# Optimization experiments

Measured on AMD Instinct MI355X. Metric: run time of the kernel, lower is better.

## Reference

```python
import jax, jax.numpy as jnp
import numpy as np

B, N, DM, H, DH, DI = 32, 512, 512, 8, 64, 2048
LEAKY_SLOPE = 0.01  # torch F.leaky_relu default
EPS = 1e-5          # torch LayerNorm default


def _ln(x, w, b):
    mu = jnp.mean(x, axis=-1, keepdims=True)
    var = jnp.var(x, axis=-1, keepdims=True)
    return (x - mu) * jax.lax.rsqrt(var + EPS) * w + b


def setup_inputs() -> dict:
    key = jax.random.key(0)
    ks = jax.random.split(key, 12)
    s = 0.02
    return {
        "Z": jax.random.normal(ks[0], (B, N, DM), jnp.float32),
        "D": jax.random.uniform(ks[1], (B, N, N), jnp.float32) * 10.0,  # pairwise distances
        "new_mask": jnp.zeros((B, N, N), jnp.float32),   # additive pre-softmax mask
        "mask": jnp.ones((B, N, N), jnp.float32),        # multiplicative post-softmax mask
        "gamma": jnp.ones((4, 4), jnp.float32),          # region-pair bias table
        "qkv_w": jax.random.normal(ks[2], (3 * DM, DM), jnp.float32) * s,
        "qkv_b": jnp.zeros((3 * DM,), jnp.float32),
        "o_w": jax.random.normal(ks[3], (DM, H * DH), jnp.float32) * s,
        "ln1_w": jnp.ones((DM,), jnp.float32),
        "ln1_b": jnp.zeros((DM,), jnp.float32),
        "ln2_w": jnp.ones((DM,), jnp.float32),
        "ln2_b": jnp.zeros((DM,), jnp.float32),
        "p1_w": jax.random.normal(ks[4], (DI, DM), jnp.float32) * s,
        "p1_b": jnp.zeros((DI,), jnp.float32),
        "p2_w": jax.random.normal(ks[5], (DM, DI), jnp.float32) * s,
        "p2_b": jnp.zeros((DM,), jnp.float32),
        "ra_end": 170,  # RA = slice(0,170), RB = slice(170,340), RT = slice(340,N)
        "rb_end": 340,
    }


def reference(Z, D, new_mask, mask, gamma, qkv_w, qkv_b, o_w,
              ln1_w, ln1_b, ln2_w, ln2_b, p1_w, p1_b, p2_w, p2_b,
              ra_end, rb_end):
    bsz, n, dm = Z.shape
    # region id per element: 0=RA, 1=RB, 2=RT (use_quad=False)
    idx = jnp.arange(n)
    region = (idx >= ra_end).astype(jnp.int32) + (idx >= rb_end).astype(jnp.int32)
    gamma_mask = gamma[region[:, None], region[None, :]]  # [N, N]

    inp = Z
    Zn = _ln(Z, ln1_w, ln1_b)
    qkv = (Zn @ qkv_w.T + qkv_b).reshape(bsz, n, H, 3 * DH)
    Z2, Z3, Z4 = jnp.split(qkv, 3, axis=3)  # V, Q, K : [B,N,H,DH]

    # scores[b,h,n,m] = -gamma*D + QK/sqrt(d) + additive mask
    scores = (-(gamma_mask[None] * D)[:, None]
              + jnp.einsum('bnhd,bmhd->bhnm', Z3, Z4) / np.sqrt(DH)
              + new_mask[:, None])
    W = jax.nn.softmax(scores, axis=3) * mask[:, None]  # post-softmax masking

    attn = jnp.einsum('bhnm,bmhd->bnhd', W, Z2).reshape(bsz, n, dm)
    attn = jax.nn.leaky_relu(attn, LEAKY_SLOPE) @ o_w.T  # o_net has no bias
    Z = attn + inp

    inp2 = Z
    Zn2 = _ln(Z, ln2_w, ln2_b)
    return jax.nn.relu(Zn2 @ p1_w.T + p1_b) @ p2_w.T + p2_b + inp2
```

## Files before the change

kernel.cpp:

```cpp
#include <hip/hip_runtime.h>
#include <hip/hip_bf16.h>

#define B_  32
#define N_  512
#define DM_ 512
#define H_  8
#define DH_ 64
#define DI_ 2048

typedef __attribute__((ext_vector_type(8))) __bf16 bf16x8;
typedef __attribute__((ext_vector_type(4))) float f32x4;
typedef __attribute__((ext_vector_type(8))) unsigned short us8;
typedef __attribute__((ext_vector_type(4))) unsigned short us4;
typedef __attribute__((ext_vector_type(4))) unsigned int u32x4;

typedef __attribute__((address_space(1))) const void g_cvoid;
typedef __attribute__((address_space(3))) void l_void;

__device__ __forceinline__ float b2f(unsigned short u) {
  union { unsigned int i; float f; } x; x.i = ((unsigned int)u) << 16; return x.f;
}
__device__ __forceinline__ unsigned short f2b(float f) {
  union { float f; unsigned int i; } x; x.f = f;
  unsigned int r = x.i + 0x7FFFu + ((x.i >> 16) & 1u);
  return (unsigned short)(r >> 16);
}
__device__ __forceinline__ void gld_lds16(const unsigned short* g, unsigned short* l) {
  __builtin_amdgcn_global_load_lds((g_cvoid*)g, (l_void*)l, 16, 0, 0);
}

__global__ __launch_bounds__(256) void prep_sm(const float* __restrict__ Dg,
                                               const float* __restrict__ nmg,
                                               const float* __restrict__ mkg,
                                               const float* __restrict__ gammaf,
                                               const int* __restrict__ ra,
                                               const int* __restrict__ rb,
                                               unsigned int* __restrict__ packed) {
  __shared__ unsigned int t[64][65];
  const int bid = blockIdx.x;
  const int kt = bid & 7, qt = (bid >> 3) & 7, b = bid >> 6;
  const int tid = threadIdx.x;
  const int ra_e = *ra, rb_e = *rb;
  const int r = tid >> 2;
  const int c = (tid & 3) * 16;
  const int q_g = qt * 64 + r;
  const int rq = (q_g >= ra_e) + (q_g >= rb_e);
  const float g0 = gammaf[rq * 4], g1 = gammaf[rq * 4 + 1], g2 = gammaf[rq * 4 + 2];
  const size_t base = ((size_t)b * N_ + q_g) * N_ + kt * 64 + c;
#pragma unroll
  for (int i = 0; i < 4; i++) {
    f32x4 dv = *(const f32x4*)(Dg + base + i * 4);
    f32x4 nv = *(const f32x4*)(nmg + base + i * 4);
    f32x4 mv = *(const f32x4*)(mkg + base + i * 4);
#pragma unroll
    for (int j = 0; j < 4; j++) {
      const int gk = kt * 64 + c + i * 4 + j;
      const float g = gk >= rb_e ? g2 : (gk >= ra_e ? g1 : g0);
      const float E = __expf(nv[j] - g * dv[j]);
      const float Em = E * mv[j];
      t[r][c + i * 4 + j] = (unsigned int)f2b(E) | ((unsigned int)f2b(Em) << 16);
    }
  }
  __syncthreads();
  const int rr = tid >> 2;
  const int cc = (tid & 3) * 16;
  unsigned int* dst = packed + ((size_t)b * N_ + kt * 64 + rr) * N_ + qt * 64 + cc;
#pragma unroll
  for (int i = 0; i < 4; i++) {
    u32x4 v;
#pragma unroll
    for (int j = 0; j < 4; j++) v[j] = t[cc + i * 4 + j][rr];
    *(u32x4*)(dst + i * 4) = v;
  }
}

__global__ __launch_bounds__(256) void conv_w(const float* __restrict__ a, const float* __restrict__ b,
                                              const float* __restrict__ c, const float* __restrict__ d,
                                              unsigned short* __restrict__ oa, unsigned short* __restrict__ ob,
                                              unsigned short* __restrict__ oc, unsigned short* __restrict__ od) {
  const int bid = blockIdx.x;
  const float* src; unsigned short* dst; int idx;
  if (bid < 384)       { src = a; dst = oa; idx = bid; }
  else if (bid < 512)  { src = b; dst = ob; idx = bid - 384; }
  else if (bid < 1024) { src = c; dst = oc; idx = bid - 512; }
  else                 { src = d; dst = od; idx = bid - 1024; }
  const int off = idx * 2048 + threadIdx.x * 8;
  f32x4 x0 = *(const f32x4*)(src + off);
  f32x4 x1 = *(const f32x4*)(src + off + 4);
  us8 o;
#pragma unroll
  for (int i = 0; i < 4; i++) { o[i] = f2b(x0[i]); o[4 + i] = f2b(x1[i]); }
  *(us8*)(dst + off) = o;
}

__global__ __launch_bounds__(256) void ln_kernel(const float* __restrict__ x,
                                                 const float* __restrict__ w,
                                                 const float* __restrict__ b,
                                                 unsigned short* __restrict__ y) {
  const int row  = blockIdx.x * 4 + (threadIdx.x >> 6);
  const int lane = threadIdx.x & 63;
  const float* xr = x + (size_t)row * DM_ + lane * 8;
  f32x4 x0 = *(const f32x4*)xr;
  f32x4 x1 = *(const f32x4*)(xr + 4);
  float v[8]; float s = 0.f;
#pragma unroll
  for (int i = 0; i < 4; i++) { v[i] = x0[i]; v[4 + i] = x1[i]; }
#pragma unroll
  for (int i = 0; i < 8; i++) s += v[i];
#pragma unroll
  for (int o = 1; o < 64; o <<= 1) s += __shfl_xor(s, o);
  const float mu = s * (1.f / DM_);
  float q = 0.f;
#pragma unroll
  for (int i = 0; i < 8; i++) { float d = v[i] - mu; q += d * d; }
#pragma unroll
  for (int o = 1; o < 64; o <<= 1) q += __shfl_xor(q, o);
  const float rstd = rsqrtf(q * (1.f / DM_) + 1e-5f);
  f32x4 w0 = *(const f32x4*)(w + lane * 8);
  f32x4 w1 = *(const f32x4*)(w + lane * 8 + 4);
  f32x4 b0 = *(const f32x4*)(b + lane * 8);
  f32x4 b1 = *(const f32x4*)(b + lane * 8 + 4);
  us8 out;
#pragma unroll
  for (int i = 0; i < 4; i++) {
    out[i]     = f2b((v[i] - mu) * rstd * w0[i] + b0[i]);
    out[4 + i] = f2b((v[4 + i] - mu) * rstd * w1[i] + b1[i]);
  }
  *(us8*)(y + (size_t)row * DM_ + lane * 8) = out;
}

struct GemmP {
  const unsigned short* A;
  const unsigned short* Bw;
  const float* bias;
  const float* residf;
  unsigned short* outb;
  float* outf;
  unsigned short* out_q;
  unsigned short* out_k;
  int K;
  int tiles_n;
  int ldo;
};

template <int EPI>
__global__ __launch_bounds__(256) void gemm_bt(GemmP p) {
  __shared__ unsigned short As[128 * 32];
  __shared__ unsigned short Bs[128 * 32];
  const int tid = threadIdx.x;
  const int wave = tid >> 6, lane = tid & 63;
  const int wm = wave >> 1, wn = wave & 1;
  const int tn = blockIdx.x % p.tiles_n, tm = blockIdx.x / p.tiles_n;
  const int K = p.K;
  const unsigned short* Ab = p.A + (size_t)tm * 128 * K;
  const unsigned short* Bb = p.Bw + (size_t)tn * 128 * K;
  f32x4 acc[4][4];
#pragma unroll
  for (int i = 0; i < 4; i++)
#pragma unroll
    for (int j = 0; j < 4; j++) acc[i][j] = (f32x4){0.f, 0.f, 0.f, 0.f};

  const int srow = lane >> 2;
  const int scol = (lane & 3) * 8;
  for (int kt = 0; kt < K; kt += 32) {
    __syncthreads();
#pragma unroll
    for (int i = 0; i < 2; i++) {
      const int r = wave * 32 + i * 16;
      gld_lds16(Ab + (size_t)(r + srow) * K + kt + scol, &As[r * 32]);
      gld_lds16(Bb + (size_t)(r + srow) * K + kt + scol, &Bs[r * 32]);
    }
    __syncthreads();
    bf16x8 af[4], bfr[4];
#pragma unroll
    for (int m = 0; m < 4; m++)
      af[m] = *(const bf16x8*)&As[(wm * 64 + m * 16 + (lane & 15)) * 32 + (lane >> 4) * 8];
#pragma unroll
    for (int n = 0; n < 4; n++)
      bfr[n] = *(const bf16x8*)&Bs[(wn * 64 + n * 16 + (lane & 15)) * 32 + (lane >> 4) * 8];
#pragma unroll
    for (int m = 0; m < 4; m++)
#pragma unroll
      for (int n = 0; n < 4; n++)
        acc[m][n] = __builtin_amdgcn_mfma_f32_16x16x32_bf16(af[m], bfr[n], acc[m][n], 0, 0, 0);
  }

  const int r0 = tm * 128 + wm * 64;
  const int c0 = tn * 128 + wn * 64;
#pragma unroll
  for (int m = 0; m < 4; m++) {
#pragma unroll
    for (int n = 0; n < 4; n++) {
#pragma unroll
      for (int rr = 0; rr < 4; rr++) {
        const int row = r0 + m * 16 + (lane >> 4) * 4 + rr;
        const int col = c0 + n * 16 + (lane & 15);
        float v = acc[m][n][rr];
        if (EPI == 0) {
          v += p.bias[col];
          const int h = col / 192, j = col % 192;
          const int bb = row >> 9, nn = row & 511;
          const size_t base = (((size_t)bb * H_ + h) * N_ + nn) * DH_;
          if (j < 64)       p.outb [base + j]        = f2b(v);
          else if (j < 128) p.out_q[base + j - 64]   = f2b(v * 0.125f);
          else              p.out_k[base + j - 128]  = f2b(v);
        } else if (EPI == 1) {
          p.outf[(size_t)row * p.ldo + col] = v + p.residf[(size_t)row * p.ldo + col];
        } else if (EPI == 2) {
          v += p.bias[col];
          v = v > 0.f ? v : 0.f;
          p.outb[(size_t)row * p.ldo + col] = f2b(v);
        } else {
          p.outf[(size_t)row * p.ldo + col] =
              v + p.bias[col] + p.residf[(size_t)row * p.ldo + col];
        }
      }
    }
  }
}

__global__ __launch_bounds__(256) void transp_v(const unsigned short* __restrict__ V,
                                                unsigned short* __restrict__ Vt) {
  __shared__ unsigned short t[64][65];
  const int bid = blockIdx.x;
  const int bh = bid >> 3, nt = bid & 7;
  const int n0 = nt * 64;
  const int tid = threadIdx.x;
  const unsigned short* src = V + ((size_t)bh * N_ + n0) * DH_;
  {
    const int r = tid >> 2, c = (tid & 3) * 16;
    us8 a = *(const us8*)(src + (size_t)r * DH_ + c);
    us8 b8 = *(const us8*)(src + (size_t)r * DH_ + c + 8);
#pragma unroll
    for (int i = 0; i < 8; i++) { t[r][c + i] = a[i]; t[r][c + 8 + i] = b8[i]; }
  }
  __syncthreads();
  {
    const int d = tid >> 2, nc = (tid & 3) * 16;
    us8 o1, o2;
#pragma unroll
    for (int i = 0; i < 8; i++) { o1[i] = t[nc + i][d]; o2[i] = t[nc + 8 + i][d]; }
    unsigned short* dst = Vt + ((size_t)bh * DH_ + d) * N_ + n0 + nc;
    *(us8*)dst = o1;
    *(us8*)(dst + 8) = o2;
  }
}

__global__ __launch_bounds__(256, 3) void attn_kernel(
    const unsigned short* __restrict__ Qs, const unsigned short* __restrict__ Ks,
    const unsigned short* __restrict__ Vt, const unsigned int* __restrict__ packed,
    unsigned short* __restrict__ attn_out) {
  __shared__ unsigned short Kt[64 * 64];
  __shared__ unsigned short Vtt[64 * 64];

  const int bid = blockIdx.x;
  const int qt = bid & 7, h = (bid >> 3) & 7, b = bid >> 6;
  const int q0 = qt * 64;
  const int tid = threadIdx.x, wave = tid >> 6, lane = tid & 63;
  const int q = lane & 15, hi = lane >> 4;

  const int q_g = q0 + wave * 16 + q;
  const size_t bh = (size_t)b * H_ + h;
  const unsigned short* Qb = Qs + (bh * N_ + q_g) * DH_;
  bf16x8 qf[2];
  qf[0] = *(const bf16x8*)(Qb + hi * 8);
  qf[1] = *(const bf16x8*)(Qb + 32 + hi * 8);

  const unsigned short* Kb = Ks + bh * N_ * DH_;
  const unsigned short* Vb = Vt + bh * DH_ * N_;
  const unsigned int* Pb = packed + (size_t)b * N_ * N_ + (size_t)(hi * 4) * N_ + q_g - wave * 16 - q
                           + (q0 + wave * 16 + q) - q0 - wave * 16 - q + q0 + wave * 16 + q;
  const unsigned int* Pbase = packed + (size_t)b * N_ * N_ + q_g;

  f32x4 o[4];
#pragma unroll
  for (int i = 0; i < 4; i++) o[i] = (f32x4){0.f, 0.f, 0.f, 0.f};
  float dsum = 0.f;

  const int str = tid >> 2;
  const int stc = tid & 3;

  us8 pk0, pk1, pv0, pv1;
  unsigned int ppw[16];

  auto load_tile = [&](int kt) {
    const unsigned short* Kp = Kb + (size_t)(kt + str) * DH_ + stc * 16;
    const unsigned short* Vp = Vb + (size_t)str * N_ + kt + stc * 16;
    pk0 = *(const us8*)Kp;
    pk1 = *(const us8*)(Kp + 8);
    pv0 = *(const us8*)Vp;
    pv1 = *(const us8*)(Vp + 8);
    const unsigned int* Pp = Pbase + (size_t)(kt + hi * 4) * N_;
#pragma unroll
    for (int c = 0; c < 4; c++)
#pragma unroll
      for (int j = 0; j < 4; j++)
        ppw[c * 4 + j] = Pp[(size_t)(c * 16 + j) * N_];
  };

  load_tile(0);

  for (int kt = 0; kt < N_; kt += 64) {
    __syncthreads();
    {
      const int c0 = (stc * 2) ^ (str & 7);
      const int c1 = (stc * 2 + 1) ^ (str & 7);
      *(us8*)&Kt[str * 64 + c0 * 8] = pk0;
      *(us8*)&Kt[str * 64 + c1 * 8] = pk1;
      *(us8*)&Vtt[str * 64 + c0 * 8] = pv0;
      *(us8*)&Vtt[str * 64 + c1 * 8] = pv1;
    }
    unsigned int cpw[16];
#pragma unroll
    for (int i = 0; i < 16; i++) cpw[i] = ppw[i];
    __syncthreads();
    if (kt + 64 < N_) load_tile(kt + 64);

    f32x4 s4[4];
#pragma unroll
    for (int c = 0; c < 4; c++) {
      f32x4 a = (f32x4){0.f, 0.f, 0.f, 0.f};
#pragma unroll
      for (int kd = 0; kd < 2; kd++) {
        const int krow = c * 16 + q;
        const int chunk = (kd * 4 + hi) ^ (q & 7);
        bf16x8 kf = *(const bf16x8*)&Kt[krow * 64 + chunk * 8];
        a = __builtin_amdgcn_mfma_f32_16x16x32_bf16(kf, qf[kd], a, 0, 0, 0);
      }
      s4[c] = a;
    }

    unsigned int pkk[4][2];
#pragma unroll
    for (int c = 0; c < 4; c++) {
      float pm[4];
#pragma unroll
      for (int r = 0; r < 4; r++) {
        const float es = __expf(s4[c][r]);
        const unsigned int w = cpw[c * 4 + r];
        dsum += es * b2f((unsigned short)(w & 0xffffu));
        pm[r] = es * b2f((unsigned short)(w >> 16));
      }
      pkk[c][0] = (unsigned int)f2b(pm[0]) | ((unsigned int)f2b(pm[1]) << 16);
      pkk[c][1] = (unsigned int)f2b(pm[2]) | ((unsigned int)f2b(pm[3]) << 16);
    }

#pragma unroll
    for (int dc = 0; dc < 4; dc++) {
      const int vrow = dc * 16 + q;
#pragma unroll
      for (int t = 0; t < 2; t++) {
        u32x4 pb = {pkk[t][0], pkk[t][1], pkk[t + 2][0], pkk[t + 2][1]};
        bf16x8 pf = __builtin_bit_cast(bf16x8, pb);
        const int ch1 = (2 * t + (hi >> 1)) ^ (vrow & 7);
        const int ch2 = (2 * t + 4 + (hi >> 1)) ^ (vrow & 7);
        us4 v1 = *(const us4*)&Vtt[vrow * 64 + ch1 * 8 + (hi & 1) * 4];
        us4 v2 = *(const us4*)&Vtt[vrow * 64 + ch2 * 8 + (hi & 1) * 4];
        us8 vv;
#pragma unroll
        for (int i = 0; i < 4; i++) { vv[i] = v1[i]; vv[4 + i] = v2[i]; }
        bf16x8 vf = __builtin_bit_cast(bf16x8, vv);
        o[dc] = __builtin_amdgcn_mfma_f32_16x16x32_bf16(vf, pf, o[dc], 0, 0, 0);
      }
    }
  }

  dsum += __shfl_xor(dsum, 16);
  dsum += __shfl_xor(dsum, 32);
  const float inv = 1.f / dsum;

  const size_t obase = ((size_t)b * N_ + q_g) * DM_ + h * DH_ + hi * 4;
#pragma unroll
  for (int dc = 0; dc < 4; dc++) {
    us4 ov;
#pragma unroll
    for (int r = 0; r < 4; r++) {
      float val = o[dc][r] * inv;
      val = val >= 0.f ? val : 0.01f * val;
      ov[r] = f2b(val);
    }
    *(us4*)&attn_out[obase + dc * 16] = ov;
  }
}

extern "C" void kernel_launch(void* const* d_in, const int* in_sizes, int n_in,
                              void* d_out, int out_size, void* d_ws, size_t ws_size,
                              hipStream_t stream) {
  const float* Z     = (const float*)d_in[0];
  const float* D     = (const float*)d_in[1];
  const float* nm    = (const float*)d_in[2];
  const float* mask  = (const float*)d_in[3];
  const float* gamma = (const float*)d_in[4];
  const float* qkv_w = (const float*)d_in[5];
  const float* qkv_b = (const float*)d_in[6];
  const float* o_w   = (const float*)d_in[7];
  const float* ln1_w = (const float*)d_in[8];
  const float* ln1_b = (const float*)d_in[9];
  const float* ln2_w = (const float*)d_in[10];
  const float* ln2_b = (const float*)d_in[11];
  const float* p1_w  = (const float*)d_in[12];
  const float* p1_b  = (const float*)d_in[13];
  const float* p2_w  = (const float*)d_in[14];
  const float* p2_b  = (const float*)d_in[15];
  const int* ra = (const int*)d_in[16];
  const int* rb = (const int*)d_in[17];
  float* out = (float*)d_out;

  const size_t SZ = (size_t)16384 * 512;
  unsigned short* buf0  = (unsigned short*)d_ws;
  unsigned short* bufQ  = buf0 + SZ;
  unsigned short* bufK  = bufQ + SZ;
  unsigned short* bufV  = bufK + SZ;
  unsigned short* bufVt = bufV + SZ;
  float* bufZ = (float*)(bufVt + SZ);
  unsigned short* bufH = bufQ;
  unsigned int* packed = (unsigned int*)bufZ;
  unsigned short* wQKV = (unsigned short*)(bufZ + SZ);
  unsigned short* wO   = wQKV + (size_t)3 * DM_ * DM_;
  unsigned short* wP1  = wO + (size_t)DM_ * DM_;
  unsigned short* wP2  = wP1 + (size_t)DI_ * DM_;

  prep_sm<<<2048, 256, 0, stream>>>(D, nm, mask, gamma, ra, rb, packed);

  conv_w<<<1536, 256, 0, stream>>>(qkv_w, o_w, p1_w, p2_w, wQKV, wO, wP1, wP2);

  ln_kernel<<<4096, 256, 0, stream>>>(Z, ln1_w, ln1_b, buf0);

  GemmP p1{};
  p1.A = buf0; p1.Bw = wQKV; p1.bias = qkv_b;
  p1.outb = bufV; p1.out_q = bufQ; p1.out_k = bufK;
  p1.K = 512; p1.tiles_n = 12; p1.ldo = 0;
  gemm_bt<0><<<128 * 12, 256, 0, stream>>>(p1);

  transp_v<<<2048, 256, 0, stream>>>(bufV, bufVt);

  attn_kernel<<<B_ * H_ * 8, 256, 0, stream>>>(bufQ, bufK, bufVt, packed, buf0);

  GemmP p3{};
  p3.A = buf0; p3.Bw = wO; p3.residf = Z; p3.outf = bufZ;
  p3.K = 512; p3.tiles_n = 4; p3.ldo = 512;
  gemm_bt<1><<<128 * 4, 256, 0, stream>>>(p3);

  ln_kernel<<<4096, 256, 0, stream>>>(bufZ, ln2_w, ln2_b, buf0);

  GemmP p5{};
  p5.A = buf0; p5.Bw = wP1; p5.bias = p1_b; p5.outb = bufH;
  p5.K = 512; p5.tiles_n = 16; p5.ldo = 2048;
  gemm_bt<2><<<128 * 16, 256, 0, stream>>>(p5);

  GemmP p6{};
  p6.A = bufH; p6.Bw = wP2; p6.bias = p2_b; p6.residf = bufZ; p6.outf = out;
  p6.K = 2048; p6.tiles_n = 4; p6.ldo = 512;
  gemm_bt<3><<<128 * 4, 256, 0, stream>>>(p6);
}
```

Measured before the change: 323.1 us.

## Double-buffer GEMM LDS staging and add XCD-aware block swizzle

The bf16 GEMM kernel now keeps two LDS buffers for the A and B tiles. It issues the global-to-LDS loads for the next K slice before running the MFMAs on the current one, and uses one barrier per iteration instead of two, so load latency overlaps with compute. Both the GEMM and attention kernels remap blockIdx so that consecutive logical tiles land on the same XCD, aiming for better L2 reuse of shared weight and K/V tiles. The swizzle assumes the grid size is a multiple of 8. The double buffer doubles GEMM shared memory, which may lower occupancy. A dead pointer computation in the attention kernel is also removed.

New measurement: 289.1 us. 10.5% less time.

```diff
diff --git a/kernel.cpp b/kernel.cpp
--- a/kernel.cpp
+++ b/kernel.cpp
@@ -27,6 +27,9 @@
 }
 __device__ __forceinline__ void gld_lds16(const unsigned short* g, unsigned short* l) {
   __builtin_amdgcn_global_load_lds((g_cvoid*)g, (l_void*)l, 16, 0, 0);
+}
+__device__ __forceinline__ int xcd_swz(int bid, int nwg) {
+  return (bid & 7) * (nwg >> 3) + (bid >> 3);
 }
 
 __global__ __launch_bounds__(256) void prep_sm(const float* __restrict__ Dg,
@@ -145,12 +148,13 @@
 
 template <int EPI>
 __global__ __launch_bounds__(256) void gemm_bt(GemmP p) {
-  __shared__ unsigned short As[128 * 32];
-  __shared__ unsigned short Bs[128 * 32];
+  __shared__ unsigned short As[2][128 * 32];
+  __shared__ unsigned short Bs[2][128 * 32];
   const int tid = threadIdx.x;
   const int wave = tid >> 6, lane = tid & 63;
   const int wm = wave >> 1, wn = wave & 1;
-  const int tn = blockIdx.x % p.tiles_n, tm = blockIdx.x / p.tiles_n;
+  const int bid = xcd_swz(blockIdx.x, gridDim.x);
+  const int tn = bid % p.tiles_n, tm = bid / p.tiles_n;
   const int K = p.K;
   const unsigned short* Ab = p.A + (size_t)tm * 128 * K;
   const unsigned short* Bb = p.Bw + (size_t)tn * 128 * K;
@@ -162,27 +166,34 @@
 
   const int srow = lane >> 2;
   const int scol = (lane & 3) * 8;
-  for (int kt = 0; kt < K; kt += 32) {
-    __syncthreads();
+  auto stage = [&](int buf, int kt) {
 #pragma unroll
     for (int i = 0; i < 2; i++) {
       const int r = wave * 32 + i * 16;
-      gld_lds16(Ab + (size_t)(r + srow) * K + kt + scol, &As[r * 32]);
-      gld_lds16(Bb + (size_t)(r + srow) * K + kt + scol, &Bs[r * 32]);
-    }
-    __syncthreads();
+      gld_lds16(Ab + (size_t)(r + srow) * K + kt + scol, &As[buf][r * 32]);
+      gld_lds16(Bb + (size_t)(r + srow) * K + kt + scol, &Bs[buf][r * 32]);
+    }
+  };
+
+  stage(0, 0);
+  __syncthreads();
+  const int nIter = K >> 5;
+  for (int it = 0; it < nIter; it++) {
+    const int buf = it & 1;
+    if (it + 1 < nIter) stage(buf ^ 1, (it + 1) * 32);
     bf16x8 af[4], bfr[4];
 #pragma unroll
     for (int m = 0; m < 4; m++)
-      af[m] = *(const bf16x8*)&As[(wm * 64 + m * 16 + (lane & 15)) * 32 + (lane >> 4) * 8];
+      af[m] = *(const bf16x8*)&As[buf][(wm * 64 + m * 16 + (lane & 15)) * 32 + (lane >> 4) * 8];
 #pragma unroll
     for (int n = 0; n < 4; n++)
-      bfr[n] = *(const bf16x8*)&Bs[(wn * 64 + n * 16 + (lane & 15)) * 32 + (lane >> 4) * 8];
+      bfr[n] = *(const bf16x8*)&Bs[buf][(wn * 64 + n * 16 + (lane & 15)) * 32 + (lane >> 4) * 8];
 #pragma unroll
     for (int m = 0; m < 4; m++)
 #pragma unroll
       for (int n = 0; n < 4; n++)
         acc[m][n] = __builtin_amdgcn_mfma_f32_16x16x32_bf16(af[m], bfr[n], acc[m][n], 0, 0, 0);
+    __syncthreads();
   }
 
   const int r0 = tm * 128 + wm * 64;
@@ -253,7 +264,7 @@
   __shared__ unsigned short Kt[64 * 64];
   __shared__ unsigned short Vtt[64 * 64];
 
-  const int bid = blockIdx.x;
+  const int bid = xcd_swz(blockIdx.x, gridDim.x);
   const int qt = bid & 7, h = (bid >> 3) & 7, b = bid >> 6;
   const int q0 = qt * 64;
   const int tid = threadIdx.x, wave = tid >> 6, lane = tid & 63;
@@ -268,8 +279,6 @@
 
   const unsigned short* Kb = Ks + bh * N_ * DH_;
   const unsigned short* Vb = Vt + bh * DH_ * N_;
-  const unsigned int* Pb = packed + (size_t)b * N_ * N_ + (size_t)(hi * 4) * N_ + q_g - wave * 16 - q
-                           + (q0 + wave * 16 + q) - q0 - wave * 16 - q + q0 + wave * 16 + q;
   const unsigned int* Pbase = packed + (size_t)b * N_ * N_ + q_g;
 
   f32x4 o[4];
```
